# Performance work log

Hardware: AMD Instinct MI355X
Metric: run time of the kernel (lower is better)

The kernel has to match this reference:

```python
import jax, jax.numpy as jnp
import numpy as np

B, T, C, HS = 4, 2048, 1024, 16
H = C // HS
LAYER_ID, N_LAYER = 2, 24
D_MIX, D_DECAY = 32, 64
LN_EPS = 1e-5


def setup_inputs() -> dict:
    key = jax.random.key(0)
    ks = jax.random.split(key, 8)
    r01 = LAYER_ID / (N_LAYER - 1)
    r10 = 1.0 - LAYER_ID / N_LAYER
    ddd = (np.arange(C, dtype=np.float64) / C)
    tm = lambda p: (1.0 - ddd ** p).reshape(1, 1, C).astype(np.float32)
    time_maa_x = tm(r10)
    time_maa_w = tm(r10)
    time_maa_k = tm(r10)
    time_maa_v = (1.0 - (ddd ** r10 + 0.3 * r01)).reshape(1, 1, C).astype(np.float32)
    time_maa_r = tm(0.5 * r10)
    n = np.arange(C, dtype=np.float64)
    decay = (-6.0 + 5.0 * (n / (C - 1)) ** (0.7 + 1.3 * r01)).reshape(1, 1, C).astype(np.float32)
    zig = ((n + 1) % 3 - 1) * 0.1
    faaaa = (r01 * (1.0 - n / (C - 1)) + zig).reshape(H, HS).astype(np.float32)
    u01 = lambda k, s: jax.random.uniform(k, s, jnp.float32, -0.01, 0.01)
    return {
        "x": jax.random.normal(ks[0], (B, T, C), jnp.float32),
        "time_maa_x": jnp.asarray(time_maa_x),
        "time_maa_w": jnp.asarray(time_maa_w),
        "time_maa_k": jnp.asarray(time_maa_k),
        "time_maa_v": jnp.asarray(time_maa_v),
        "time_maa_r": jnp.asarray(time_maa_r),
        "time_maa_w1": u01(ks[1], (C, D_MIX * 4)),
        "time_maa_w2": u01(ks[2], (4, D_MIX, C)),
        "time_decay": jnp.asarray(decay),
        "time_decay_w1": u01(ks[3], (C, D_DECAY)),
        "time_decay_w2": u01(ks[4], (D_DECAY, C)),
        "time_faaaa": jnp.asarray(faaaa),
        "W_r": jax.random.normal(ks[5], (C, C), jnp.float32) * 0.02,
        "W_k": jax.random.normal(ks[6], (C, C), jnp.float32) * 0.02,
        "W_v": jax.random.normal(ks[7], (C, C), jnp.float32) * 0.02,
        "W_o": jax.random.normal(jax.random.fold_in(key, 99), (C, C), jnp.float32) * 0.02,
        "ln_g": jnp.ones((C,), jnp.float32),
        "ln_b": jnp.zeros((C,), jnp.float32),
    }


def _wkv6(r, k, v, w, u):
    # r,k,v,w: [B,T,H,N]; u: [H,N]. Per-head 16x16 state, rank-1 updates.
    wd = jnp.exp(-jnp.exp(w))  # decay in (0,1)
    rT, kT, vT, wT = (a.transpose(1, 0, 2, 3) for a in (r, k, v, wd))  # [T,B,H,N]

    def step(S, ins):
        r_t, k_t, v_t, w_t = ins  # each [B,H,N]
        kv = jnp.einsum("bhi,bhj->bhij", k_t, v_t)
        y_t = jnp.einsum("bhi,bhij->bhj", r_t, S + u[None, :, :, None] * kv)
        return w_t[..., None] * S + kv, y_t

    S0 = jnp.zeros((r.shape[0], H, HS, HS), r.dtype)
    _, ys = jax.lax.scan(step, S0, (rT, kT, vT, wT))  # ys: [T,B,H,N]
    return ys.transpose(1, 0, 2, 3)


def reference(x, time_maa_x, time_maa_w, time_maa_k, time_maa_v, time_maa_r,
              time_maa_w1, time_maa_w2, time_decay, time_decay_w1, time_decay_w2,
              time_faaaa, W_r, W_k, W_v, W_o, ln_g, ln_b):
    b, t, c = x.shape
    # time shift: previous token (zero at t=0)
    xx = jnp.concatenate([jnp.zeros_like(x[:, :1]), x[:, :-1]], axis=1) - x
    xxx = x + xx * time_maa_x
    m = jnp.tanh(xxx @ time_maa_w1).reshape(b, t, 4, D_MIX)
    m = jnp.einsum("btfd,fdc->fbtc", m, time_maa_w2)  # [4,B,T,C]
    mw, mk, mv, mr = m[0], m[1], m[2], m[3]
    xw = x + xx * (time_maa_w + mw)
    xk = x + xx * (time_maa_k + mk)
    xv = x + xx * (time_maa_v + mv)
    xr = x + xx * (time_maa_r + mr)
    r = (xr @ W_r).reshape(b, t, H, HS)
    k = (xk @ W_k).reshape(b, t, H, HS)
    v = (xv @ W_v).reshape(b, t, H, HS)
    ww = jnp.tanh(xw @ time_decay_w1) @ time_decay_w2
    w = (time_decay + ww).reshape(b, t, H, HS)
    y = _wkv6(r, k, v, w, time_faaaa).reshape(b, t, c)
    mu = jnp.mean(y, axis=-1, keepdims=True)
    var = jnp.mean(jnp.square(y - mu), axis=-1, keepdims=True)
    y = (y - mu) * jax.lax.rsqrt(var + LN_EPS) * ln_g + ln_b
    return y @ W_o
```

## Files before the change

### kernel.cpp

```cpp
#include <hip/hip_runtime.h>
#include <stdint.h>

#define TT 2048
#define CC 1024

typedef short bf16x8 __attribute__((ext_vector_type(8)));
typedef float f32x4 __attribute__((ext_vector_type(4)));
typedef unsigned uint2v __attribute__((ext_vector_type(2)));
typedef __attribute__((address_space(3))) uint32_t lds_u32_t;
typedef const __attribute__((address_space(1))) uint32_t glb_u32_t;

__device__ inline unsigned short f2b(float f) {
  union { float f; unsigned u; } c; c.f = f;
  unsigned u = c.u;
  return (unsigned short)((u + 0x7fffu + ((u >> 16) & 1u)) >> 16);
}
__device__ inline float b2f(unsigned short s) {
  union { unsigned u; float f; } c; c.u = ((unsigned)s) << 16; return c.f;
}

__device__ inline void gl_lds16(const void* g, void* l) {
  glb_u32_t* gp = (glb_u32_t*)(uintptr_t)g;
  lds_u32_t* lp = (lds_u32_t*)(uint32_t)(uintptr_t)l;
  __builtin_amdgcn_global_load_lds(gp, lp, 16, 0, 0);
}

__device__ inline void swiz(int& bx, int& by, int& bz) {
  int nx = gridDim.x, ny = gridDim.y;
  int flat = (blockIdx.z * ny + blockIdx.y) * nx + blockIdx.x;
  int xcd = flat & 7;
  int idx = flat >> 3;
  int perz = (nx * ny) >> 3;
  bz = idx / perz;
  int rem = idx - bz * perz;
  int r = rem / nx;
  bx = rem - r * nx;
  by = xcd * (ny >> 3) + r;
}

struct TSeg { const float* in; unsigned short* out; int R, C, tx, start; };
struct TransAll { TSeg seg[11]; int nseg; };
__global__ void transpose_all(TransAll ta) {
  __shared__ float tile[32][33];
  int bid = blockIdx.x;
  int si = 0;
  while (si + 1 < ta.nseg && bid >= ta.seg[si + 1].start) si++;
  TSeg sg = ta.seg[si];
  int lt = bid - sg.start;
  int bx = lt % sg.tx, by = lt / sg.tx;
  int c0 = bx * 32, r0 = by * 32;
  int tx = threadIdx.x, ty = threadIdx.y;
  for (int i = ty; i < 32; i += 8) {
    int r = r0 + i, c = c0 + tx;
    tile[i][tx] = (r < sg.R && c < sg.C) ? sg.in[(size_t)r * sg.C + c] : 0.f;
  }
  __syncthreads();
  int rr = r0 + tx;
  for (int i = ty; i < 32; i += 8) {
    int cc = c0 + i;
    if (cc < sg.C && rr < sg.R) sg.out[(size_t)cc * sg.R + rr] = f2b(tile[tx][i]);
  }
}

__global__ void shift_mix(const float* __restrict__ x, const float* __restrict__ tmx,
                          unsigned short* __restrict__ xb, unsigned short* __restrict__ xxb,
                          unsigned short* __restrict__ xxx) {
  int idx = blockIdx.x * 256 + threadIdx.x;
  int c4 = idx & 255;
  int row = idx >> 8;
  int t = row & (TT - 1);
  const float4* x4 = (const float4*)x;
  float4 xv = x4[idx];
  float4 pv = make_float4(0.f, 0.f, 0.f, 0.f);
  if (t > 0) pv = x4[idx - 256];
  float4 d;
  d.x = pv.x - xv.x; d.y = pv.y - xv.y; d.z = pv.z - xv.z; d.w = pv.w - xv.w;
  ushort4 ob;
  ob.x = f2b(xv.x); ob.y = f2b(xv.y); ob.z = f2b(xv.z); ob.w = f2b(xv.w);
  ((ushort4*)xb)[idx] = ob;
  ushort4 od;
  od.x = f2b(d.x); od.y = f2b(d.y); od.z = f2b(d.z); od.w = f2b(d.w);
  ((ushort4*)xxb)[idx] = od;
  float4 tm = ((const float4*)tmx)[c4];
  ushort4 o;
  o.x = f2b(xv.x + d.x * tm.x);
  o.y = f2b(xv.y + d.y * tm.y);
  o.z = f2b(xv.z + d.z * tm.z);
  o.w = f2b(xv.w + d.w * tm.w);
  ((ushort4*)xxx)[idx] = o;
}

__device__ __forceinline__ void gemm_core_pipe(
    const unsigned short* __restrict__ A, const unsigned short* __restrict__ Bt,
    int k0beg, int k0end, int lda, int ldb, int rowBase, int colBase,
    unsigned short* As, unsigned short* Bs, f32x4 acc[4][4], int w, int lane,
    int quad, int l16, int waveM, int waveN) {
#pragma unroll
  for (int i = 0; i < 4; i++)
#pragma unroll
    for (int j = 0; j < 4; j++) acc[i][j] = (f32x4){0.f, 0.f, 0.f, 0.f};
  const int SSB = 8192;
  const int nIter = (k0end - k0beg) >> 5;
  int rl = lane >> 2;
  int cl = (lane & 3) ^ ((lane >> 3) & 3);
  int rA0 = w * 16 + rl, rA1 = (w + 4) * 16 + rl;
  const unsigned short* gA0 = A + (size_t)(rowBase + rA0) * lda + cl * 8 + k0beg;
  const unsigned short* gA1 = A + (size_t)(rowBase + rA1) * lda + cl * 8 + k0beg;
  const unsigned short* gB0 = Bt + (size_t)(colBase + rA0) * ldb + cl * 8 + k0beg;
  const unsigned short* gB1 = Bt + (size_t)(colBase + rA1) * ldb + cl * 8 + k0beg;
  char* dA0 = (char*)As + w * 1024;
  char* dA1 = (char*)As + (w + 4) * 1024;
  char* dB0 = (char*)Bs + w * 1024;
  char* dB1 = (char*)Bs + (w + 4) * 1024;
  int sw = quad ^ ((l16 >> 1) & 3);
  int aoff = (waveM + l16) * 64 + sw * 16;
  int boff = (waveN + l16) * 64 + sw * 16;

#define ISSUE(it, st)                               \
  {                                                 \
    int ko = (it) * 32;                             \
    gl_lds16(gA0 + ko, dA0 + (st) * SSB);           \
    gl_lds16(gA1 + ko, dA1 + (st) * SSB);           \
    gl_lds16(gB0 + ko, dB0 + (st) * SSB);           \
    gl_lds16(gB1 + ko, dB1 + (st) * SSB);           \
  }

  ISSUE(0, 0)
  if (nIter > 1) ISSUE(1, 1)
  int stage = 0;
  for (int it = 0; it < nIter; ++it) {
    if (it + 1 < nIter) {
      asm volatile("s_waitcnt vmcnt(4)\ns_barrier" ::: "memory");
    } else {
      asm volatile("s_waitcnt vmcnt(0)\ns_barrier" ::: "memory");
    }
    if (it + 2 < nIter) {
      int ns = stage + 2; if (ns >= 3) ns -= 3;
      ISSUE(it + 2, ns)
    }
    const char* Ab = (const char*)As + stage * SSB;
    const char* Bb = (const char*)Bs + stage * SSB;
    bf16x8 af[4], bfr[4];
#pragma unroll
    for (int mt = 0; mt < 4; mt++)
      af[mt] = *(const bf16x8*)(Ab + aoff + mt * 1024);
#pragma unroll
    for (int nt = 0; nt < 4; nt++)
      bfr[nt] = *(const bf16x8*)(Bb + boff + nt * 1024);
#pragma unroll
    for (int mt = 0; mt < 4; mt++)
#pragma unroll
      for (int nt = 0; nt < 4; nt++)
        acc[mt][nt] = __builtin_amdgcn_mfma_f32_16x16x32_bf16(af[mt], bfr[nt], acc[mt][nt], 0, 0, 0);
    stage = stage + 1; if (stage >= 3) stage -= 3;
  }
#undef ISSUE
}

__global__ __launch_bounds__(256) void gemm_bf16(
    const unsigned short* __restrict__ A, const unsigned short* __restrict__ Bt,
    int N, int K, int lda, int ldb, int mode, int ldc,
    float* __restrict__ outF, unsigned short* __restrict__ outB,
    const float* __restrict__ tm) {
  __shared__ __align__(16) unsigned short As[3 * 4096];
  __shared__ __align__(16) unsigned short Bs[3 * 4096];
  int bx, by, bz;
  swiz(bx, by, bz);
  (void)bz;
  int tid = threadIdx.x;
  int w = tid >> 6, lane = tid & 63;
  int quad = lane >> 4, l16 = lane & 15;
  int rowBase = by * 128;
  int colBase = bx * 128;
  int waveM = (w >> 1) * 64, waveN = (w & 1) * 64;
  f32x4 acc[4][4];
  gemm_core_pipe(A, Bt, 0, K, lda, ldb, rowBase, colBase, As, Bs, acc, w, lane, quad, l16, waveM, waveN);
#pragma unroll
  for (int mt = 0; mt < 4; mt++)
#pragma unroll
    for (int nt = 0; nt < 4; nt++)
#pragma unroll
      for (int rg = 0; rg < 4; rg++) {
        int row = rowBase + waveM + mt * 16 + quad * 4 + rg;
        int col = colBase + waveN + nt * 16 + l16;
        if (col >= N) continue;
        float val = acc[mt][nt][rg];
        if (mode == 0) {
          outF[(size_t)row * ldc + col] = val;
        } else {
          int b = row >> 11, t = row & (TT - 1), h = col >> 4, n = col & 15;
          outF[(size_t)((b * 64 + h) * TT + t) * 16 + n] = expf(-expf(tm[col] + val));
        }
      }
}

__global__ __launch_bounds__(256) void gemm_splitk(
    const unsigned short* __restrict__ A, const unsigned short* __restrict__ Bt,
    int N, int Kc, int lda, int ldb, int ldp, float* __restrict__ part) {
  __shared__ __align__(16) unsigned short As[3 * 4096];
  __shared__ __align__(16) unsigned short Bs[3 * 4096];
  int s = blockIdx.x, by = blockIdx.y;
  int M = gridDim.y * 128;
  int tid = threadIdx.x;
  int w = tid >> 6, lane = tid & 63;
  int quad = lane >> 4, l16 = lane & 15;
  int rowBase = by * 128;
  int waveM = (w >> 1) * 64, waveN = (w & 1) * 64;
  f32x4 acc[4][4];
  gemm_core_pipe(A, Bt, s * Kc, (s + 1) * Kc, lda, ldb, rowBase, 0, As, Bs, acc, w, lane, quad, l16, waveM, waveN);
  float* pb = part + (size_t)s * M * ldp;
#pragma unroll
  for (int mt = 0; mt < 4; mt++)
#pragma unroll
    for (int nt = 0; nt < 4; nt++)
#pragma unroll
      for (int rg = 0; rg < 4; rg++) {
        int row = rowBase + waveM + mt * 16 + quad * 4 + rg;
        int col = waveN + nt * 16 + l16;
        if (col < N) pb[(size_t)row * ldp + col] = acc[mt][nt][rg];
      }
}

__global__ __launch_bounds__(256) void reduce_tanh(
    const float* __restrict__ part, unsigned short* __restrict__ out,
    int total4, int S, int strideElems) {
  int idx = blockIdx.x * 256 + threadIdx.x;
  if (idx >= total4) return;
  float4 a = ((const float4*)part)[idx];
  for (int s = 1; s < S; s++) {
    float4 b = ((const float4*)(part + (size_t)s * strideElems))[idx];
    a.x += b.x; a.y += b.y; a.z += b.z; a.w += b.w;
  }
  ushort4 o;
  o.x = f2b(tanhf(a.x)); o.y = f2b(tanhf(a.y));
  o.z = f2b(tanhf(a.z)); o.w = f2b(tanhf(a.w));
  ((ushort4*)out)[idx] = o;
}

struct GateArgs {
  const unsigned short* A;
  const unsigned short* Bt;
  unsigned short* out[4];
  const float* tm[4];
  const unsigned short* xb;
  const unsigned short* xxb;
};
__global__ __launch_bounds__(256) void gemm_gate4(GateArgs ga) {
  __shared__ __align__(16) unsigned short As[3 * 4096];
  __shared__ __align__(16) unsigned short Bs[3 * 4096];
  int flat = (blockIdx.z * 64 + blockIdx.y) * 8 + blockIdx.x;
  int xcd = flat & 7;
  int idx = flat >> 3;
  int z = idx & 3;
  int tile = idx >> 2;
  int by = xcd * 8 + (tile >> 3);
  int bx = tile & 7;
  const unsigned short* A = ga.A + z * 32;
  const unsigned short* Bt = ga.Bt + (size_t)z * 1024 * 32;
  unsigned short* outB = ga.out[z];
  const float* tm = ga.tm[z];
  int tid = threadIdx.x;
  int w = tid >> 6, lane = tid & 63;
  int quad = lane >> 4, l16 = lane & 15;
  int rowBase = by * 128;
  int colBase = bx * 128;
  int waveM = (w >> 1) * 64, waveN = (w & 1) * 64;
  f32x4 acc[4][4];
  gemm_core_pipe(A, Bt, 0, 32, 128, 32, rowBase, colBase, As, Bs, acc, w, lane, quad, l16, waveM, waveN);
#pragma unroll
  for (int mt = 0; mt < 4; mt++)
#pragma unroll
    for (int nt = 0; nt < 4; nt++)
#pragma unroll
      for (int rg = 0; rg < 4; rg++) {
        int row = rowBase + waveM + mt * 16 + quad * 4 + rg;
        int col = colBase + waveN + nt * 16 + l16;
        size_t o = (size_t)row * CC + col;
        float xv = b2f(ga.xb[o]), xxv = b2f(ga.xxb[o]);
        outB[o] = f2b(xv + xxv * (tm[col] + acc[mt][nt][rg]));
      }
}

template <int NSLOT>
__device__ __forceinline__ void core256x128(
    const unsigned short* __restrict__ A, const unsigned short* __restrict__ Bt,
    int rowBase, int colBase, unsigned short* As, unsigned short* Bs,
    f32x4 acc[4][4]) {
  int tid = threadIdx.x;
  int w = tid >> 6, lane = tid & 63;
  int quad = lane >> 4, l16 = lane & 15;
  int wr = w >> 1, wc = w & 1;
  int rl = lane >> 2;
  int cl = (lane & 3) ^ ((lane >> 3) & 3);
  const unsigned short* gA0 = A + (size_t)(rowBase + w * 16 + rl) * 1024 + cl * 8;
  const unsigned short* gA1 = A + (size_t)(rowBase + (w + 8) * 16 + rl) * 1024 + cl * 8;
  const unsigned short* gB0 = Bt + (size_t)(colBase + w * 16 + rl) * 1024 + cl * 8;
  char* dA0 = (char*)As + w * 1024;
  char* dA1 = (char*)As + (w + 8) * 1024;
  char* dB0 = (char*)Bs + w * 1024;
  int sw = quad ^ ((l16 >> 1) & 3);
  int aoffB = wr * 4096 + l16 * 64 + sw * 16;
  int boffB = wc * 4096 + l16 * 64 + sw * 16;
#pragma unroll
  for (int i = 0; i < 4; i++)
#pragma unroll
    for (int j = 0; j < 4; j++) acc[i][j] = (f32x4){0.f, 0.f, 0.f, 0.f};

#define STG(h, st)                                        \
  { int kc = (h) * 32;                                    \
    int slA = (st) * 16384, slB = (st) * 8192;            \
    gl_lds16(gA0 + kc, dA0 + slA);                        \
    gl_lds16(gA1 + kc, dA1 + slA);                        \
    gl_lds16(gB0 + kc, dB0 + slB); }

  if constexpr (NSLOT == 4) {
    STG(0, 0) STG(1, 1) STG(2, 2)
    asm volatile("s_waitcnt vmcnt(6)\ns_barrier" ::: "memory");
  } else {
    STG(0, 0) STG(1, 1)
    asm volatile("s_waitcnt vmcnt(3)\ns_barrier" ::: "memory");
  }

  int sl = 0;
  for (int h = 0; h < 32; ++h) {
    const char* Ab = (const char*)As + sl * 16384;
    const char* Bb = (const char*)Bs + sl * 8192;
    bf16x8 af[4], bfr[4];
#pragma unroll
    for (int nt = 0; nt < 4; nt++)
      bfr[nt] = *(const bf16x8*)(Bb + boffB + nt * 1024);
#pragma unroll
    for (int mt = 0; mt < 4; mt++)
      af[mt] = *(const bf16x8*)(Ab + aoffB + mt * 1024);
    if (h + NSLOT - 1 < 32) {
      int ns = sl + NSLOT - 1; if (ns >= NSLOT) ns -= NSLOT;
      STG(h + NSLOT - 1, ns)
    }
    __builtin_amdgcn_s_setprio(1);
#pragma unroll
    for (int mt = 0; mt < 4; mt++)
#pragma unroll
      for (int nt = 0; nt < 4; nt++)
        acc[mt][nt] = __builtin_amdgcn_mfma_f32_16x16x32_bf16(af[mt], bfr[nt], acc[mt][nt], 0, 0, 0);
    __builtin_amdgcn_s_setprio(0);
    if constexpr (NSLOT == 4) {
      if (h <= 28) {
        asm volatile("s_waitcnt vmcnt(6) lgkmcnt(0)\ns_barrier" ::: "memory");
      } else if (h == 29) {
        asm volatile("s_waitcnt vmcnt(3) lgkmcnt(0)\ns_barrier" ::: "memory");
      } else if (h == 30) {
        asm volatile("s_waitcnt vmcnt(0) lgkmcnt(0)\ns_barrier" ::: "memory");
      }
    } else {
      if (h <= 29) {
        asm volatile("s_waitcnt vmcnt(3) lgkmcnt(0)\ns_barrier" ::: "memory");
      } else if (h == 30) {
        asm volatile("s_waitcnt vmcnt(0) lgkmcnt(0)\ns_barrier" ::: "memory");
      }
    }
    sl = sl + 1; if (sl >= NSLOT) sl = 0;
  }
#undef STG
}

struct ProjArgs {
  const unsigned short* A[3];
  const unsigned short* Bt[3];
  unsigned short* out[3];
};
__global__ __launch_bounds__(512, 4) void gemm_proj3_8ph(ProjArgs pa) {
  __shared__ __align__(16) unsigned short As[3 * 8192];
  __shared__ __align__(16) unsigned short Bs[3 * 4096];
  int bx, by, bz;
  swiz(bx, by, bz);
  f32x4 acc[4][4];
  core256x128<3>(pa.A[bz], pa.Bt[bz], by * 256, bx * 128, As, Bs, acc);
  unsigned short* outB = pa.out[bz];
  int tid = threadIdx.x;
  int w = tid >> 6, lane = tid & 63;
  int quad = lane >> 4, l16 = lane & 15;
  int wr = w >> 1, wc = w & 1;
#pragma unroll
  for (int mt = 0; mt < 4; mt++)
#pragma unroll
    for (int nt = 0; nt < 4; nt++)
#pragma unroll
      for (int rg = 0; rg < 4; rg++) {
        int row = by * 256 + wr * 64 + mt * 16 + quad * 4 + rg;
        int col = bx * 128 + wc * 64 + nt * 16 + l16;
        int b = row >> 11, t = row & (TT - 1), hh = col >> 4, n = col & 15;
        outB[(size_t)((b * 64 + hh) * TT + t) * 16 + n] = f2b(acc[mt][nt][rg]);
      }
}

__global__ __launch_bounds__(512, 2) void gemm_wo_8ph(
    const unsigned short* __restrict__ A, const unsigned short* __restrict__ Bt,
    float* __restrict__ outF) {
  __shared__ __align__(16) unsigned short As[4 * 8192];
  __shared__ __align__(16) unsigned short Bs[4 * 4096];
  int bx, by, bz;
  swiz(bx, by, bz);
  (void)bz;
  f32x4 acc[4][4];
  core256x128<4>(A, Bt, by * 256, bx * 128, As, Bs, acc);
  int tid = threadIdx.x;
  int w = tid >> 6, lane = tid & 63;
  int quad = lane >> 4, l16 = lane & 15;
  int wr = w >> 1, wc = w & 1;
#pragma unroll
  for (int mt = 0; mt < 4; mt++)
#pragma unroll
    for (int nt = 0; nt < 4; nt++)
#pragma unroll
      for (int rg = 0; rg < 4; rg++) {
        int row = by * 256 + wr * 64 + mt * 16 + quad * 4 + rg;
        int col = bx * 128 + wc * 64 + nt * 16 + l16;
        outF[(size_t)row * CC + col] = acc[mt][nt][rg];
      }
}

__device__ __forceinline__ float reduce_p(float part) {
#if __has_builtin(__builtin_amdgcn_permlane32_swap) && __has_builtin(__builtin_amdgcn_permlane16_swap)
  uint2v a = __builtin_amdgcn_permlane32_swap(__float_as_uint(part), __float_as_uint(part), false, false);
  float s1 = part + __uint_as_float(a.y);
  uint2v b = __builtin_amdgcn_permlane16_swap(__float_as_uint(s1), __float_as_uint(s1), false, false);
  return s1 + __uint_as_float(b.y);
#else
  part += __shfl_xor(part, 16, 64);
  part += __shfl_xor(part, 32, 64);
  return part;
#endif
}

__global__ __launch_bounds__(1024) void wkv_scan2(
    const unsigned short* __restrict__ r, const unsigned short* __restrict__ k,
    const unsigned short* __restrict__ v, const float* __restrict__ wd,
    const float* __restrict__ u, unsigned short* __restrict__ y) {
  __shared__ __align__(16) unsigned short lrb[16][256];
  __shared__ __align__(16) unsigned short lkb[16][256];
  __shared__ __align__(16) unsigned short lvb[16][256];
  __shared__ __align__(16) float lw[16][256];
  __shared__ __align__(16) float Lend[16][256];
  __shared__ __align__(16) float Sini[16][256];
  __shared__ float Eend[16][16];
  int bh = blockIdx.x;
  int b = bh >> 6, h = bh & 63;
  int tid = threadIdx.x;
  int c = tid >> 6, lane = tid & 63;
  int j = lane & 15, p = lane >> 4;
  size_t base = (size_t)bh * TT * 16 + (size_t)c * 128 * 16;

  float S0 = 0.f, S1 = 0.f, S2 = 0.f, S3 = 0.f;
  float E0 = 1.f, E1 = 1.f, E2 = 1.f, E3 = 1.f;
  for (int t0 = 0; t0 < 128; t0 += 16) {
    size_t off = base + (size_t)t0 * 16;
    ushort4 kv4 = ((const ushort4*)(k + off))[lane];
    ushort4 vv = ((const ushort4*)(v + off))[lane];
    float4 wv = ((const float4*)(wd + off))[lane];
    ((ushort4*)lkb[c])[lane] = kv4;
    ((ushort4*)lvb[c])[lane] = vv;
    ((float4*)lw[c])[lane] = wv;
#pragma unroll
    for (int s = 0; s < 16; s++) {
      ushort4 kk = *(const ushort4*)(lkb[c] + s * 16 + p * 4);
      float4 ww = *(const float4*)(lw[c] + s * 16 + p * 4);
      float vj = b2f(lvb[c][s * 16 + j]);
      S0 = fmaf(ww.x, S0, b2f(kk.x) * vj); E0 *= ww.x;
      S1 = fmaf(ww.y, S1, b2f(kk.y) * vj); E1 *= ww.y;
      S2 = fmaf(ww.z, S2, b2f(kk.z) * vj); E2 *= ww.z;
      S3 = fmaf(ww.w, S3, b2f(kk.w) * vj); E3 *= ww.w;
    }
  }
  Lend[c][(p * 4 + 0) * 16 + j] = S0;
  Lend[c][(p * 4 + 1) * 16 + j] = S1;
  Lend[c][(p * 4 + 2) * 16 + j] = S2;
  Lend[c][(p * 4 + 3) * 16 + j] = S3;
  if (j == 0) {
    Eend[c][p * 4 + 0] = E0;
    Eend[c][p * 4 + 1] = E1;
    Eend[c][p * 4 + 2] = E2;
    Eend[c][p * 4 + 3] = E3;
  }
  __syncthreads();

  if (c == 0) {
    float T0 = 0.f, T1 = 0.f, T2 = 0.f, T3 = 0.f;
    for (int cc = 0; cc < 16; cc++) {
      Sini[cc][(p * 4 + 0) * 16 + j] = T0;
      Sini[cc][(p * 4 + 1) * 16 + j] = T1;
      Sini[cc][(p * 4 + 2) * 16 + j] = T2;
      Sini[cc][(p * 4 + 3) * 16 + j] = T3;
      float e0 = Eend[cc][p * 4 + 0], e1 = Eend[cc][p * 4 + 1];
      float e2 = Eend[cc][p * 4 + 2], e3 = Eend[cc][p * 4 + 3];
      T0 = fmaf(e0, T0, Lend[cc][(p * 4 + 0) * 16 + j]);
      T1 = fmaf(e1, T1, Lend[cc][(p * 4 + 1) * 16 + j]);
      T2 = fmaf(e2, T2, Lend[cc][(p * 4 + 2) * 16 + j]);
      T3 = fmaf(e3, T3, Lend[cc][(p * 4 + 3) * 16 + j]);
    }
  }
  __syncthreads();

  float u0 = u[h * 16 + p * 4 + 0], u1 = u[h * 16 + p * 4 + 1];
  float u2 = u[h * 16 + p * 4 + 2], u3 = u[h * 16 + p * 4 + 3];
  S0 = Sini[c][(p * 4 + 0) * 16 + j];
  S1 = Sini[c][(p * 4 + 1) * 16 + j];
  S2 = Sini[c][(p * 4 + 2) * 16 + j];
  S3 = Sini[c][(p * 4 + 3) * 16 + j];
  for (int t0 = 0; t0 < 128; t0 += 16) {
    size_t off = base + (size_t)t0 * 16;
    ushort4 rv = ((const ushort4*)(r + off))[lane];
    ushort4 kv4 = ((const ushort4*)(k + off))[lane];
    ushort4 vv = ((const ushort4*)(v + off))[lane];
    float4 wv = ((const float4*)(wd + off))[lane];
    ((ushort4*)lrb[c])[lane] = rv;
    ((ushort4*)lkb[c])[lane] = kv4;
    ((ushort4*)lvb[c])[lane] = vv;
    ((float4*)lw[c])[lane] = wv;
#pragma unroll
    for (int s = 0; s < 16; s++) {
      ushort4 rr4 = *(const ushort4*)(lrb[c] + s * 16 + p * 4);
      ushort4 kk4 = *(const ushort4*)(lkb[c] + s * 16 + p * 4);
      float4 ww = *(const float4*)(lw[c] + s * 16 + p * 4);
      float vj = b2f(lvb[c][s * 16 + j]);
      float kv, part;
      kv = b2f(kk4.x) * vj; part = b2f(rr4.x) * fmaf(u0, kv, S0); S0 = fmaf(ww.x, S0, kv);
      kv = b2f(kk4.y) * vj; part = fmaf(b2f(rr4.y), fmaf(u1, kv, S1), part); S1 = fmaf(ww.y, S1, kv);
      kv = b2f(kk4.z) * vj; part = fmaf(b2f(rr4.z), fmaf(u2, kv, S2), part); S2 = fmaf(ww.z, S2, kv);
      kv = b2f(kk4.w) * vj; part = fmaf(b2f(rr4.w), fmaf(u3, kv, S3), part); S3 = fmaf(ww.w, S3, kv);
      float tot = reduce_p(part);
      if (p == 0) y[(size_t)(b * TT + c * 128 + t0 + s) * CC + h * 16 + j] = f2b(tot);
    }
  }
}

__global__ __launch_bounds__(256) void ln_fused(const unsigned short* __restrict__ y,
                                                const float* __restrict__ g,
                                                const float* __restrict__ be,
                                                unsigned short* __restrict__ out) {
  int row = blockIdx.x;
  int tid = threadIdx.x;
  ushort4 vb = ((const ushort4*)(y + (size_t)row * CC))[tid];
  float4 val = make_float4(b2f(vb.x), b2f(vb.y), b2f(vb.z), b2f(vb.w));
  float s = val.x + val.y + val.z + val.w;
  float sq = val.x * val.x + val.y * val.y + val.z * val.z + val.w * val.w;
#pragma unroll
  for (int m = 1; m < 64; m <<= 1) {
    s += __shfl_xor(s, m, 64);
    sq += __shfl_xor(sq, m, 64);
  }
  __shared__ float ss[4], s2[4];
  int w = tid >> 6;
  if ((tid & 63) == 0) { ss[w] = s; s2[w] = sq; }
  __syncthreads();
  s = ss[0] + ss[1] + ss[2] + ss[3];
  sq = s2[0] + s2[1] + s2[2] + s2[3];
  float mu = s * (1.f / 1024.f);
  float var = sq * (1.f / 1024.f) - mu * mu;
  float rstd = rsqrtf(var + 1e-5f);
  float4 gg = ((const float4*)g)[tid];
  float4 bb = ((const float4*)be)[tid];
  ushort4 o;
  o.x = f2b((val.x - mu) * rstd * gg.x + bb.x);
  o.y = f2b((val.y - mu) * rstd * gg.y + bb.y);
  o.z = f2b((val.z - mu) * rstd * gg.z + bb.z);
  o.w = f2b((val.w - mu) * rstd * gg.w + bb.w);
  ((ushort4*)(out + (size_t)row * CC))[tid] = o;
}

extern "C" void kernel_launch(void* const* d_in, const int* in_sizes, int n_in,
                              void* d_out, int out_size, void* d_ws, size_t ws_size,
                              hipStream_t stream) {
  (void)in_sizes; (void)n_in; (void)out_size; (void)ws_size;
  const float* x = (const float*)d_in[0];
  const float* tmx = (const float*)d_in[1];
  const float* tmw = (const float*)d_in[2];
  const float* tmk = (const float*)d_in[3];
  const float* tmv = (const float*)d_in[4];
  const float* tmr = (const float*)d_in[5];
  const float* w1 = (const float*)d_in[6];
  const float* w2 = (const float*)d_in[7];
  const float* tdecay = (const float*)d_in[8];
  const float* dw1 = (const float*)d_in[9];
  const float* dw2 = (const float*)d_in[10];
  const float* faaaa = (const float*)d_in[11];
  const float* Wr = (const float*)d_in[12];
  const float* Wk = (const float*)d_in[13];
  const float* Wv = (const float*)d_in[14];
  const float* Wo = (const float*)d_in[15];
  const float* lng = (const float*)d_in[16];
  const float* lnb = (const float*)d_in[17];
  float* out = (float*)d_out;

  char* ws = (char*)d_ws;
  const size_t MBy = 1ull << 20;
  unsigned short* rb   = (unsigned short*)(ws + 0);
  unsigned short* kbuf = (unsigned short*)(ws + 16 * MBy);
  unsigned short* vbuf = (unsigned short*)(ws + 32 * MBy);
  float* wdb = (float*)(ws + 48 * MBy);
  unsigned short* xb    = (unsigned short*)(ws + 80 * MBy);
  unsigned short* xxb16 = (unsigned short*)(ws + 96 * MBy);
  unsigned short* yb16 = (unsigned short*)(ws + 80 * MBy);
  unsigned short* xxxb = (unsigned short*)(ws + 112 * MBy);
  unsigned short* xwb  = (unsigned short*)(ws + 112 * MBy);
  unsigned short* xrb  = (unsigned short*)(ws + 128 * MBy);
  unsigned short* xkb  = (unsigned short*)(ws + 144 * MBy);
  unsigned short* ynb  = (unsigned short*)(ws + 144 * MBy);
  unsigned short* xvb  = (unsigned short*)(ws + 160 * MBy);
  float* mixP  = (float*)(ws + 128 * MBy);
  float* decP  = (float*)(ws + 0);
  unsigned short* mtmpb = (unsigned short*)(ws + 176 * MBy);
  unsigned short* dtmpb = (unsigned short*)(ws + 178 * MBy);
  char* wreg = ws + 179 * MBy;
  unsigned short* w1t  = (unsigned short*)(wreg);
  unsigned short* w2t  = (unsigned short*)(wreg + 256 * 1024);
  unsigned short* dw1t = (unsigned short*)(wreg + 512 * 1024);
  unsigned short* dw2t = (unsigned short*)(wreg + 768 * 1024);
  unsigned short* Wrt  = (unsigned short*)(wreg + 1024 * 1024);
  unsigned short* Wkt = Wrt + 1024 * 1024;
  unsigned short* Wvt = Wkt + 1024 * 1024;
  unsigned short* Wot = Wvt + 1024 * 1024;

  dim3 tb(32, 8);
  {
    TransAll ta;
    int st = 0, si = 0;
    auto add = [&](const float* in, unsigned short* o, int R, int C) {
      int tx = (C + 31) / 32, ty = (R + 31) / 32;
      ta.seg[si++] = TSeg{in, o, R, C, tx, st};
      st += tx * ty;
    };
    add(Wr, Wrt, 1024, 1024);
    add(Wk, Wkt, 1024, 1024);
    add(Wv, Wvt, 1024, 1024);
    add(Wo, Wot, 1024, 1024);
    for (int g = 0; g < 4; g++)
      add(w2 + (size_t)g * 32 * 1024, w2t + (size_t)g * 1024 * 32, 32, 1024);
    add(w1, w1t, 1024, 128);
    add(dw1, dw1t, 1024, 64);
    add(dw2, dw2t, 64, 1024);
    ta.nseg = si;
    transpose_all<<<st, tb, 0, stream>>>(ta);
  }

  shift_mix<<<8192, 256, 0, stream>>>(x, tmx, xb, xxb16, xxxb);

  gemm_splitk<<<dim3(4, 64), 256, 0, stream>>>(xxxb, w1t, 128, 256, 1024, 1024, 128, mixP);
  reduce_tanh<<<1024, 256, 0, stream>>>(mixP, mtmpb, 8192 * 128 / 4, 4, 8192 * 128);

  {
    GateArgs ga;
    ga.A = mtmpb; ga.Bt = w2t;
    ga.out[0] = xwb; ga.out[1] = xkb; ga.out[2] = xvb; ga.out[3] = xrb;
    ga.tm[0] = tmw; ga.tm[1] = tmk; ga.tm[2] = tmv; ga.tm[3] = tmr;
    ga.xb = xb; ga.xxb = xxb16;
    gemm_gate4<<<dim3(8, 64, 4), 256, 0, stream>>>(ga);
  }
  gemm_splitk<<<dim3(4, 64), 256, 0, stream>>>(xwb, dw1t, 64, 256, 1024, 1024, 64, decP);
  reduce_tanh<<<512, 256, 0, stream>>>(decP, dtmpb, 8192 * 64 / 4, 4, 8192 * 64);
  gemm_bf16<<<dim3(8, 64), 256, 0, stream>>>(dtmpb, dw2t, 1024, 64, 64, 64, 4, 1024,
                                             wdb, nullptr, tdecay);
  {
    ProjArgs pa;
    pa.A[0] = xrb; pa.A[1] = xkb; pa.A[2] = xvb;
    pa.Bt[0] = Wrt; pa.Bt[1] = Wkt; pa.Bt[2] = Wvt;
    pa.out[0] = rb; pa.out[1] = kbuf; pa.out[2] = vbuf;
    gemm_proj3_8ph<<<dim3(8, 32, 3), 512, 0, stream>>>(pa);
  }

  wkv_scan2<<<256, 1024, 0, stream>>>(rb, kbuf, vbuf, wdb, faaaa, yb16);
  ln_fused<<<8192, 256, 0, stream>>>(yb16, lng, lnb, ynb);
  gemm_wo_8ph<<<dim3(8, 32), 512, 0, stream>>>(ynb, Wot, out);
}
```

Baseline: 362.9 us.

## Split WKV chunked scan into three kernels with more chunks per head

Replaces the single 1024-thread block per (batch, head) scan with three launches: a chunk-local state pass, a per-head prefix over chunk end states, and an output pass seeded with the prefix states. The number of chunks doubles from 16 to 32 and each wave becomes an independent task in 256-thread blocks, which shortens the serial per-wave chain and raises occupancy. The cost is two extra launches and global round trips for the chunk states and decay products in place of shared memory. The prefix kernel also runs a serial loop over 32 chunks.

```diff
diff --git a/kernel.cpp b/kernel.cpp
--- a/kernel.cpp
+++ b/kernel.cpp
@@ -3,6 +3,7 @@
 
 #define TT 2048
 #define CC 1024
+#define NCH 32
 
 typedef short bf16x8 __attribute__((ext_vector_type(8)));
 typedef float f32x4 __attribute__((ext_vector_type(4)));
@@ -432,103 +433,108 @@
 #endif
 }
 
-__global__ __launch_bounds__(1024) void wkv_scan2(
-    const unsigned short* __restrict__ r, const unsigned short* __restrict__ k,
-    const unsigned short* __restrict__ v, const float* __restrict__ wd,
-    const float* __restrict__ u, unsigned short* __restrict__ y) {
-  __shared__ __align__(16) unsigned short lrb[16][256];
-  __shared__ __align__(16) unsigned short lkb[16][256];
-  __shared__ __align__(16) unsigned short lvb[16][256];
-  __shared__ __align__(16) float lw[16][256];
-  __shared__ __align__(16) float Lend[16][256];
-  __shared__ __align__(16) float Sini[16][256];
-  __shared__ float Eend[16][16];
-  int bh = blockIdx.x;
-  int b = bh >> 6, h = bh & 63;
-  int tid = threadIdx.x;
-  int c = tid >> 6, lane = tid & 63;
+__global__ __launch_bounds__(256, 8) void wkv_p1(
+    const unsigned short* __restrict__ k, const unsigned short* __restrict__ v,
+    const float* __restrict__ wd, float* __restrict__ Lg, float* __restrict__ Eg) {
+  __shared__ __align__(16) unsigned short lkb[4][256];
+  __shared__ __align__(16) unsigned short lvb[4][256];
+  __shared__ __align__(16) float lw[4][256];
+  int tid = threadIdx.x;
+  int wl = tid >> 6, lane = tid & 63;
+  int task = blockIdx.x * 4 + wl;
   int j = lane & 15, p = lane >> 4;
-  size_t base = (size_t)bh * TT * 16 + (size_t)c * 128 * 16;
+  size_t base = (size_t)task * (TT / NCH) * 16;
 
   float S0 = 0.f, S1 = 0.f, S2 = 0.f, S3 = 0.f;
   float E0 = 1.f, E1 = 1.f, E2 = 1.f, E3 = 1.f;
-  for (int t0 = 0; t0 < 128; t0 += 16) {
+  for (int t0 = 0; t0 < TT / NCH; t0 += 16) {
     size_t off = base + (size_t)t0 * 16;
-    ushort4 kv4 = ((const ushort4*)(k + off))[lane];
-    ushort4 vv = ((const ushort4*)(v + off))[lane];
-    float4 wv = ((const float4*)(wd + off))[lane];
-    ((ushort4*)lkb[c])[lane] = kv4;
-    ((ushort4*)lvb[c])[lane] = vv;
-    ((float4*)lw[c])[lane] = wv;
+    ((ushort4*)lkb[wl])[lane] = ((const ushort4*)(k + off))[lane];
+    ((ushort4*)lvb[wl])[lane] = ((const ushort4*)(v + off))[lane];
+    ((float4*)lw[wl])[lane] = ((const float4*)(wd + off))[lane];
 #pragma unroll
     for (int s = 0; s < 16; s++) {
-      ushort4 kk = *(const ushort4*)(lkb[c] + s * 16 + p * 4);
-      float4 ww = *(const float4*)(lw[c] + s * 16 + p * 4);
-      float vj = b2f(lvb[c][s * 16 + j]);
+      ushort4 kk = *(const ushort4*)(lkb[wl] + s * 16 + p * 4);
+      float4 ww = *(const float4*)(lw[wl] + s * 16 + p * 4);
+      float vj = b2f(lvb[wl][s * 16 + j]);
       S0 = fmaf(ww.x, S0, b2f(kk.x) * vj); E0 *= ww.x;
       S1 = fmaf(ww.y, S1, b2f(kk.y) * vj); E1 *= ww.y;
       S2 = fmaf(ww.z, S2, b2f(kk.z) * vj); E2 *= ww.z;
       S3 = fmaf(ww.w, S3, b2f(kk.w) * vj); E3 *= ww.w;
     }
   }
-  Lend[c][(p * 4 + 0) * 16 + j] = S0;
-  Lend[c][(p * 4 + 1) * 16 + j] = S1;
-  Lend[c][(p * 4 + 2) * 16 + j] = S2;
-  Lend[c][(p * 4 + 3) * 16 + j] = S3;
+  float* Lt = Lg + (size_t)task * 256;
+  Lt[(p * 4 + 0) * 16 + j] = S0;
+  Lt[(p * 4 + 1) * 16 + j] = S1;
+  Lt[(p * 4 + 2) * 16 + j] = S2;
+  Lt[(p * 4 + 3) * 16 + j] = S3;
   if (j == 0) {
-    Eend[c][p * 4 + 0] = E0;
-    Eend[c][p * 4 + 1] = E1;
-    Eend[c][p * 4 + 2] = E2;
-    Eend[c][p * 4 + 3] = E3;
-  }
-  __syncthreads();
-
-  if (c == 0) {
-    float T0 = 0.f, T1 = 0.f, T2 = 0.f, T3 = 0.f;
-    for (int cc = 0; cc < 16; cc++) {
-      Sini[cc][(p * 4 + 0) * 16 + j] = T0;
-      Sini[cc][(p * 4 + 1) * 16 + j] = T1;
-      Sini[cc][(p * 4 + 2) * 16 + j] = T2;
-      Sini[cc][(p * 4 + 3) * 16 + j] = T3;
-      float e0 = Eend[cc][p * 4 + 0], e1 = Eend[cc][p * 4 + 1];
-      float e2 = Eend[cc][p * 4 + 2], e3 = Eend[cc][p * 4 + 3];
-      T0 = fmaf(e0, T0, Lend[cc][(p * 4 + 0) * 16 + j]);
-      T1 = fmaf(e1, T1, Lend[cc][(p * 4 + 1) * 16 + j]);
-      T2 = fmaf(e2, T2, Lend[cc][(p * 4 + 2) * 16 + j]);
-      T3 = fmaf(e3, T3, Lend[cc][(p * 4 + 3) * 16 + j]);
-    }
-  }
-  __syncthreads();
+    float* Et = Eg + (size_t)task * 16;
+    Et[p * 4 + 0] = E0;
+    Et[p * 4 + 1] = E1;
+    Et[p * 4 + 2] = E2;
+    Et[p * 4 + 3] = E3;
+  }
+}
+
+__global__ __launch_bounds__(256) void wkv_prefix(
+    const float* __restrict__ Lg, const float* __restrict__ Eg,
+    float* __restrict__ Sini) {
+  int bh = blockIdx.x;
+  int tid = threadIdx.x;
+  int i = tid >> 4, j = tid & 15;
+  float T = 0.f;
+  for (int cc = 0; cc < NCH; ++cc) {
+    size_t tk = (size_t)bh * NCH + cc;
+    Sini[tk * 256 + i * 16 + j] = T;
+    T = fmaf(Eg[tk * 16 + i], T, Lg[tk * 256 + i * 16 + j]);
+  }
+}
+
+__global__ __launch_bounds__(256, 8) void wkv_p2(
+    const unsigned short* __restrict__ r, const unsigned short* __restrict__ k,
+    const unsigned short* __restrict__ v, const float* __restrict__ wd,
+    const float* __restrict__ u, const float* __restrict__ Sini,
+    unsigned short* __restrict__ y) {
+  __shared__ __align__(16) unsigned short lrb[4][256];
+  __shared__ __align__(16) unsigned short lkb[4][256];
+  __shared__ __align__(16) unsigned short lvb[4][256];
+  __shared__ __align__(16) float lw[4][256];
+  int tid = threadIdx.x;
+  int wl = tid >> 6, lane = tid & 63;
+  int task = blockIdx.x * 4 + wl;
+  int bh = task >> 5, c = task & (NCH - 1);
+  int b = bh >> 6, h = bh & 63;
+  int j = lane & 15, p = lane >> 4;
+  size_t base = (size_t)task * (TT / NCH) * 16;
 
   float u0 = u[h * 16 + p * 4 + 0], u1 = u[h * 16 + p * 4 + 1];
   float u2 = u[h * 16 + p * 4 + 2], u3 = u[h * 16 + p * 4 + 3];
-  S0 = Sini[c][(p * 4 + 0) * 16 + j];
-  S1 = Sini[c][(p * 4 + 1) * 16 + j];
-  S2 = Sini[c][(p * 4 + 2) * 16 + j];
-  S3 = Sini[c][(p * 4 + 3) * 16 + j];
-  for (int t0 = 0; t0 < 128; t0 += 16) {
+  const float* Sv = Sini + (size_t)task * 256;
+  float S0 = Sv[(p * 4 + 0) * 16 + j];
+  float S1 = Sv[(p * 4 + 1) * 16 + j];
+  float S2 = Sv[(p * 4 + 2) * 16 + j];
+  float S3 = Sv[(p * 4 + 3) * 16 + j];
+  for (int t0 = 0; t0 < TT / NCH; t0 += 16) {
     size_t off = base + (size_t)t0 * 16;
-    ushort4 rv = ((const ushort4*)(r + off))[lane];
-    ushort4 kv4 = ((const ushort4*)(k + off))[lane];
-    ushort4 vv = ((const ushort4*)(v + off))[lane];
-    float4 wv = ((const float4*)(wd + off))[lane];
-    ((ushort4*)lrb[c])[lane] = rv;
-    ((ushort4*)lkb[c])[lane] = kv4;
-    ((ushort4*)lvb[c])[lane] = vv;
-    ((float4*)lw[c])[lane] = wv;
+    ((ushort4*)lrb[wl])[lane] = ((const ushort4*)(r + off))[lane];
+    ((ushort4*)lkb[wl])[lane] = ((const ushort4*)(k + off))[lane];
+    ((ushort4*)lvb[wl])[lane] = ((const ushort4*)(v + off))[lane];
+    ((float4*)lw[wl])[lane] = ((const float4*)(wd + off))[lane];
 #pragma unroll
     for (int s = 0; s < 16; s++) {
-      ushort4 rr4 = *(const ushort4*)(lrb[c] + s * 16 + p * 4);
-      ushort4 kk4 = *(const ushort4*)(lkb[c] + s * 16 + p * 4);
-      float4 ww = *(const float4*)(lw[c] + s * 16 + p * 4);
-      float vj = b2f(lvb[c][s * 16 + j]);
+      ushort4 rr4 = *(const ushort4*)(lrb[wl] + s * 16 + p * 4);
+      ushort4 kk4 = *(const ushort4*)(lkb[wl] + s * 16 + p * 4);
+      float4 ww = *(const float4*)(lw[wl] + s * 16 + p * 4);
+      float vj = b2f(lvb[wl][s * 16 + j]);
       float kv, part;
       kv = b2f(kk4.x) * vj; part = b2f(rr4.x) * fmaf(u0, kv, S0); S0 = fmaf(ww.x, S0, kv);
       kv = b2f(kk4.y) * vj; part = fmaf(b2f(rr4.y), fmaf(u1, kv, S1), part); S1 = fmaf(ww.y, S1, kv);
       kv = b2f(kk4.z) * vj; part = fmaf(b2f(rr4.z), fmaf(u2, kv, S2), part); S2 = fmaf(ww.z, S2, kv);
       kv = b2f(kk4.w) * vj; part = fmaf(b2f(rr4.w), fmaf(u3, kv, S3), part); S3 = fmaf(ww.w, S3, kv);
       float tot = reduce_p(part);
-      if (p == 0) y[(size_t)(b * TT + c * 128 + t0 + s) * CC + h * 16 + j] = f2b(tot);
+      if (p == 0)
+        y[(size_t)(b * TT + c * (TT / NCH) + t0 + s) * CC + h * 16 + j] = f2b(tot);
     }
   }
 }
@@ -608,6 +614,9 @@
   unsigned short* xvb  = (unsigned short*)(ws + 160 * MBy);
   float* mixP  = (float*)(ws + 128 * MBy);
   float* decP  = (float*)(ws + 0);
+  float* Lg   = (float*)(ws + 128 * MBy);
+  float* SinG = (float*)(ws + 136 * MBy);
+  float* Eg   = (float*)(ws + 144 * MBy);
   unsigned short* mtmpb = (unsigned short*)(ws + 176 * MBy);
   unsigned short* dtmpb = (unsigned short*)(ws + 178 * MBy);
   char* wreg = ws + 179 * MBy;
@@ -667,7 +676,10 @@
     gemm_proj3_8ph<<<dim3(8, 32, 3), 512, 0, stream>>>(pa);
   }
 
-  wkv_scan2<<<256, 1024, 0, stream>>>(rb, kbuf, vbuf, wdb, faaaa, yb16);
+  wkv_p1<<<2048, 256, 0, stream>>>(kbuf, vbuf, wdb, Lg, Eg);
+  wkv_prefix<<<256, 256, 0, stream>>>(Lg, Eg, SinG);
+  wkv_p2<<<2048, 256, 0, stream>>>(rb, kbuf, vbuf, wdb, faaaa, SinG, yb16);
+
   ln_fused<<<8192, 256, 0, stream>>>(yb16, lng, lnb, ynb);
   gemm_wo_8ph<<<dim3(8, 32), 512, 0, stream>>>(ynb, Wot, out);
 }
```

Result: slower. 450.0 us (+24.0%).
